# Kernel tuning notes

Hardware: AMD Instinct MI355X
Metric: run time of the kernel (lower is better)

Reference implementation:

```python
import jax, jax.numpy as jnp
import numpy as np

N_CELLS = 50000
HID = 64
DEG = 16
K_NODES = 4  # nodes per cell; cell i owns nodes [4i, 4i+4)
SP = 3


def setup_inputs() -> dict:
    key = jax.random.key(0)
    ks = jax.random.split(key, 12)
    s = 1.0 / np.sqrt(HID)
    inp = {
        'features': jax.random.normal(ks[0], (N_CELLS, HID), jnp.float32),
        'positions': jax.random.normal(ks[1], (K_NODES * N_CELLS, SP), jnp.float32),
        'neighbors': jax.random.randint(ks[2], (N_CELLS, DEG), 0, N_CELLS, jnp.int32),
        # message MLP: Linear(2H+1 -> H), SiLU, Linear(H -> H)
        'W1': jax.random.normal(ks[3], (2 * HID + 1, HID), jnp.float32) * s,
        'b1': jnp.zeros((HID,), jnp.float32),
        'W2': jax.random.normal(ks[4], (HID, HID), jnp.float32) * s,
        'b2': jnp.zeros((HID,), jnp.float32),
        # update MLP: Linear(H + H -> H), SiLU, Linear(H -> H)
        'Wu1': jax.random.normal(ks[5], (2 * HID, HID), jnp.float32) * s,
        'bu1': jnp.zeros((HID,), jnp.float32),
        'Wu2': jax.random.normal(ks[6], (HID, HID), jnp.float32) * s,
        'bu2': jnp.zeros((HID,), jnp.float32),
    }
    return inp


def reference(features, positions, neighbors, W1, b1, W2, b2, Wu1, bu1, Wu2, bu2):
    N, H = features.shape
    # centroid of each cell's owned nodes (cell i -> nodes [K*i, K*i+K))
    cent = positions.reshape(N, K_NODES, SP).mean(axis=1)          # [N, sp]
    fj = features[neighbors]                                       # [N, D, H]
    cj = cent[neighbors]                                           # [N, D, sp]
    # centroid-distance geometric invariant per (cell, neighbor) pair
    geom = jnp.linalg.norm(cent[:, None, :] - cj, axis=-1, keepdims=True)  # [N, D, 1]
    fi = jnp.broadcast_to(features[:, None, :], fj.shape)          # [N, D, H]
    x = jnp.concatenate([fi, fj, geom], axis=-1)                   # [N, D, 2H+1]
    h = jax.nn.silu(x @ W1 + b1) @ W2 + b2                         # [N, D, H]
    msg = h.mean(axis=1)                                           # mean over neighbors
    u = jnp.concatenate([features, msg], axis=-1)                  # [N, 2H]
    upd = jax.nn.silu(u @ Wu1 + bu1) @ Wu2 + bu2
    updated_features = features + upd
    return updated_features, positions
```

## Files before the change

kernel.cpp:

```cpp
#include <hip/hip_runtime.h>


#define DEG 16

typedef __attribute__((ext_vector_type(8))) short short8;
typedef __attribute__((ext_vector_type(4))) float f32x4;
typedef uint2 uint2_a __attribute__((may_alias));
typedef uint4 uint4_a __attribute__((may_alias));
typedef unsigned short ushort_a __attribute__((may_alias));

union HbRd { uint4_a u; short8 s; };
union Frag { short8 s; uint4 u; };

__device__ __forceinline__ unsigned f2bf(float f) {
  unsigned u = __float_as_uint(f);
  return (u + 0x7FFFu + ((u >> 16) & 1u)) >> 16;
}
__device__ __forceinline__ float bf2f(unsigned bits16) {
  return __uint_as_float(bits16 << 16);
}
__device__ __forceinline__ float silu(float h) {
  return h / (1.f + __expf(-h));
}
__device__ __forceinline__ float silu_fast(float h) {
  return h * __builtin_amdgcn_rcpf(1.f + __expf(-h));
}

__global__ __launch_bounds__(256) void prep_aux_kernel(
    const float* __restrict__ feat,
    const float* __restrict__ pos,
    const float* __restrict__ W1, const float* __restrict__ W2,
    const float* __restrict__ Wu1, const float* __restrict__ Wu2,
    float* __restrict__ outpos, float* __restrict__ cent4,
    unsigned short* __restrict__ w1pq, unsigned short* __restrict__ w2t,
    unsigned short* __restrict__ wu1t, unsigned short* __restrict__ wu2b,
    unsigned char* __restrict__ Q8)
{
  __shared__ unsigned short w1q[4096];

  if (blockIdx.x < 782) {
    const int tid  = threadIdx.x;
    const int lane = tid & 63;
    const int wid  = tid >> 6;
    const int quad = lane >> 4;
    const int l15  = lane & 15;

    {
      const int q  = (tid >> 3) & 3;
      const int kk = (tid >> 5) & 1;
      const int mq = tid >> 6;
      #pragma unroll
      for (int u = 0; u < 2; ++u) {
        const int l = (tid * 2 + u) & 15;
        const float* src = W1 + (64 + kk * 32 + q * 8) * 64 + mq * 16 + l;
        unsigned short v[8];
        #pragma unroll
        for (int j = 0; j < 8; ++j)
          v[j] = (unsigned short)f2bf(src[j * 64]);
        uint4 pk;
        pk.x = (unsigned)v[0] | ((unsigned)v[1] << 16);
        pk.y = (unsigned)v[2] | ((unsigned)v[3] << 16);
        pk.z = (unsigned)v[4] | ((unsigned)v[5] << 16);
        pk.w = (unsigned)v[6] | ((unsigned)v[7] << 16);
        ((uint4*)w1q)[tid * 2 + u] = pk;
      }
    }

    const int tile = blockIdx.x * 4 + wid;
    const bool act = (tile < 3125);
    const int  tt  = act ? tile : 3124;
    const int  cr  = tt * 16 + l15;

    short8 xf[2];
    #pragma unroll
    for (int kk = 0; kk < 2; ++kk) {
      const float4 f0 = *(const float4*)(feat + cr * 64 + kk * 32 + quad * 8);
      const float4 f1 = *(const float4*)(feat + cr * 64 + kk * 32 + quad * 8 + 4);
      Frag v;
      v.s[0] = (short)f2bf(f0.x); v.s[1] = (short)f2bf(f0.y);
      v.s[2] = (short)f2bf(f0.z); v.s[3] = (short)f2bf(f0.w);
      v.s[4] = (short)f2bf(f1.x); v.s[5] = (short)f2bf(f1.y);
      v.s[6] = (short)f2bf(f1.z); v.s[7] = (short)f2bf(f1.w);
      xf[kk] = v.s;
    }

    __syncthreads();

    short8 wf[4][2];
    #pragma unroll
    for (int m = 0; m < 4; ++m)
      #pragma unroll
      for (int kk = 0; kk < 2; ++kk)
        wf[m][kk] = *(const short8*)(w1q + (((m * 2 + kk) * 4 + quad) << 7) + l15 * 8);

    f32x4 acc[4] = {};
    #pragma unroll
    for (int kk = 0; kk < 2; ++kk)
      #pragma unroll
      for (int m = 0; m < 4; ++m)
        acc[m] = __builtin_amdgcn_mfma_f32_16x16x32_bf16(wf[m][kk], xf[kk], acc[m], 0, 0, 0);

    if (act) {
      #pragma unroll
      for (int m = 0; m < 4; ++m) {
        int w = __builtin_amdgcn_cvt_pk_fp8_f32(acc[m][0], acc[m][1], 0, false);
        w = __builtin_amdgcn_cvt_pk_fp8_f32(acc[m][2], acc[m][3], w, true);
        *(unsigned int*)(Q8 + cr * 64 + m * 16 + quad * 4) = (unsigned)w;
      }
    }
  } else {
    const int t = (blockIdx.x - 782) * 256 + threadIdx.x;
    if (t < 150000) {
      ((float4*)outpos)[t] = ((const float4*)pos)[t];
    } else if (t < 174576) {
      const int r = t - 150000;
      if (r < 8192) {
        const int j = r & 7, l = (r >> 3) & 15, q = (r >> 7) & 3;
        const int f = r >> 9, kk = f & 1, mt = f >> 1;
        const int k = kk * 32 + q * 8 + j;
        const int m = mt * 16 + l;
        w1pq[r] = (unsigned short)f2bf(
            (m < 64) ? W1[k * 64 + m] : W1[(k + 64) * 64 + (m - 64)]);
      } else if (r < 12288) {
        const int s = r - 8192;
        const int j = s & 7, l = (s >> 3) & 15, q = (s >> 7) & 3;
        const int f = s >> 9, kk = f & 1, mt = f >> 1;
        const int k = kk * 32 + q * 8 + j;
        w2t[s] = (unsigned short)f2bf(W2[k * 64 + mt * 16 + l]);
      } else if (r < 20480) {
        const int s = r - 12288;
        const int j = s & 7, l = (s >> 3) & 15, q = (s >> 7) & 3;
        const int f = s >> 9, kk = f & 3, mt = f >> 2;
        const int k = kk * 32 + q * 8 + j;
        wu1t[s] = (unsigned short)f2bf(Wu1[k * 64 + mt * 16 + l]);
      } else {
        const int s = r - 20480;
        const int j = s & 7, l = (s >> 3) & 15, q = (s >> 7) & 3;
        const int f = s >> 9, kk = f & 1, nt = f >> 1;
        const int k = kk * 32 + q * 8 + j;
        wu2b[s] = (unsigned short)f2bf(Wu2[k * 64 + nt * 16 + l]);
      }
    } else if (t < 224576) {
      const int i = t - 174576;
      const float4* pp = (const float4*)(pos + 12 * i);
      const float4 a = pp[0], b = pp[1], c = pp[2];
      float4 o;
      o.x = (a.x + a.w + b.z + c.y) * 0.25f;
      o.y = (a.y + b.x + b.w + c.z) * 0.25f;
      o.z = (a.z + b.y + c.x + c.w) * 0.25f;
      o.w = 0.f;
      ((float4*)cent4)[i] = o;
    }
  }
}

__global__ __launch_bounds__(256) void msg_tail_kernel(
    const unsigned char* __restrict__ Q8,
    const float4* __restrict__ cent4,
    const int* __restrict__ nbr,
    const float* __restrict__ feat,
    const unsigned short* __restrict__ w1pq,
    const unsigned short* __restrict__ w2t,
    const unsigned short* __restrict__ wu1t,
    const unsigned short* __restrict__ wu2b,
    const float* __restrict__ b1, const float* __restrict__ W1,
    const float* __restrict__ b2, const float* __restrict__ bu1,
    const float* __restrict__ bu2,
    float* __restrict__ outf)
{
  __shared__ uint4 smem[432];
  char* sT  = (char*)smem;
  char* Msg = sT + 2304;
  char* Hb  = sT + 4608;

  const int lane = threadIdx.x & 63;
  const int wid  = threadIdx.x >> 6;
  const int quad = lane >> 4;
  const int l15  = lane & 15;
  const int tile = blockIdx.x;
  const int cr   = tile * 16 + l15;

  const float b1l = b1[lane];
  const float wl  = W1[8192 + lane];

  int nj[4];
  #pragma unroll
  for (int i = 0; i < 4; ++i) {
    const int cs = __builtin_amdgcn_readfirstlane(tile * 16 + wid * 4 + i);
    nj[i] = nbr[cs * DEG + l15];
  }
  float g[4];
  #pragma unroll
  for (int i = 0; i < 4; ++i) {
    const int cs = __builtin_amdgcn_readfirstlane(tile * 16 + wid * 4 + i);
    const float4 ci = cent4[cs];
    const float4 cj = cent4[nj[i]];
    const float dx = ci.x - cj.x, dy = ci.y - cj.y, dz = ci.z - cj.z;
    g[i] = sqrtf(dx * dx + dy * dy + dz * dz);
  }

  Frag xf[2];
  #pragma unroll
  for (int kk = 0; kk < 2; ++kk) {
    const float4 f0 = *(const float4*)(feat + cr * 64 + kk * 32 + quad * 8);
    const float4 f1 = *(const float4*)(feat + cr * 64 + kk * 32 + quad * 8 + 4);
    Frag v;
    v.s[0] = (short)f2bf(f0.x); v.s[1] = (short)f2bf(f0.y);
    v.s[2] = (short)f2bf(f0.z); v.s[3] = (short)f2bf(f0.w);
    v.s[4] = (short)f2bf(f1.x); v.s[5] = (short)f2bf(f1.y);
    v.s[6] = (short)f2bf(f1.z); v.s[7] = (short)f2bf(f1.w);
    xf[kk] = v;
  }

  {
    short8 wpf[2];
    #pragma unroll
    for (int kk = 0; kk < 2; ++kk)
      wpf[kk] = *(const short8*)(w1pq + (((wid * 2 + kk) * 4 + quad) << 7) + l15 * 8);
    f32x4 accp = {};
    #pragma unroll
    for (int kk = 0; kk < 2; ++kk)
      accp = __builtin_amdgcn_mfma_f32_16x16x32_bf16(wpf[kk], xf[kk].s, accp, 0, 0, 0);
    uint2 pk;
    pk.x = f2bf(accp[0]) | (f2bf(accp[1]) << 16);
    pk.y = f2bf(accp[2]) | (f2bf(accp[3]) << 16);
    *(uint2_a*)(sT + l15 * 144 + wid * 32 + quad * 8) = pk;
  }

  unsigned qA[16], qB[16];
  #pragma unroll
  for (int d = 0; d < 16; ++d) {
    const int nd = __builtin_amdgcn_readlane(nj[0], d);
    qA[d] = Q8[nd * 64 + lane];
  }

  __syncthreads();

  #pragma unroll
  for (int i = 0; i < 4; ++i) {
    unsigned (&qc)[16] = (i & 1) ? qB : qA;
    unsigned (&qn)[16] = (i & 1) ? qA : qB;
    if (i < 3) {
      #pragma unroll
      for (int d = 0; d < 16; ++d) {
        const int nd = __builtin_amdgcn_readlane(nj[i + 1], d);
        qn[d] = Q8[nd * 64 + lane];
      }
    }
    const float pcb =
        bf2f(((const ushort_a*)(sT + (wid * 4 + i) * 144))[lane]) + b1l;
    float acc = 0.f;
    #pragma unroll
    for (int d = 0; d < 16; ++d) {
      const float gd = __uint_as_float(
          __builtin_amdgcn_readlane((int)__float_as_uint(g[i]), d));
      const float qv = __builtin_amdgcn_cvt_f32_fp8((int)qc[d], 0);
      acc += silu_fast(pcb + qv + gd * wl);
    }
    ((ushort_a*)(sT + (wid * 4 + i) * 144))[lane] =
        (unsigned short)f2bf(acc * 0.0625f);
  }

  short8 w2f[2], wu1f[4], wu2f[2];
  #pragma unroll
  for (int kk = 0; kk < 2; ++kk)
    w2f[kk]  = *(const short8*)(w2t  + (((wid * 2 + kk) * 4 + quad) << 7) + l15 * 8);
  #pragma unroll
  for (int kk = 0; kk < 4; ++kk)
    wu1f[kk] = *(const short8*)(wu1t + (((wid * 4 + kk) * 4 + quad) << 7) + l15 * 8);
  #pragma unroll
  for (int kk = 0; kk < 2; ++kk)
    wu2f[kk] = *(const short8*)(wu2b + (((wid * 2 + kk) * 4 + quad) << 7) + l15 * 8);

  const f32x4 b2f  = *(const f32x4*)(b2  + wid * 16 + quad * 4);
  const f32x4 bu1f = *(const f32x4*)(bu1 + wid * 16 + quad * 4);
  const float bu2v = bu2[wid * 16 + l15];

  __syncthreads();

  f32x4 accm = {};
  #pragma unroll
  for (int kk = 0; kk < 2; ++kk) {
    HbRd t; t.u = *(const uint4_a*)(sT + l15 * 144 + kk * 64 + quad * 16);
    accm = __builtin_amdgcn_mfma_f32_16x16x32_bf16(w2f[kk], t.s, accm, 0, 0, 0);
  }
  {
    uint2 pk;
    pk.x = f2bf(accm[0] + b2f[0]) | (f2bf(accm[1] + b2f[1]) << 16);
    pk.y = f2bf(accm[2] + b2f[2]) | (f2bf(accm[3] + b2f[3]) << 16);
    *(uint2_a*)(Msg + l15 * 144 + wid * 32 + quad * 8) = pk;
  }
  __syncthreads();

  f32x4 accu = {};
  #pragma unroll
  for (int kk = 0; kk < 4; ++kk) {
    short8 bf;
    if (kk < 2) {
      bf = xf[kk].s;
    } else {
      HbRd t; t.u = *(const uint4_a*)(Msg + l15 * 144 + (kk - 2) * 64 + quad * 16);
      bf = t.s;
    }
    accu = __builtin_amdgcn_mfma_f32_16x16x32_bf16(wu1f[kk], bf, accu, 0, 0, 0);
  }
  {
    float sv[4];
    #pragma unroll
    for (int rg = 0; rg < 4; ++rg)
      sv[rg] = silu(accu[rg] + bu1f[rg]);
    uint2 pk;
    pk.x = f2bf(sv[0]) | (f2bf(sv[1]) << 16);
    pk.y = f2bf(sv[2]) | (f2bf(sv[3]) << 16);
    *(uint2_a*)(Hb + l15 * 144 + wid * 32 + quad * 8) = pk;
  }
  __syncthreads();

  f32x4 acc2 = {};
  #pragma unroll
  for (int kk = 0; kk < 2; ++kk) {
    HbRd t; t.u = *(const uint4_a*)(Hb + l15 * 144 + kk * 64 + quad * 16);
    acc2 = __builtin_amdgcn_mfma_f32_16x16x32_bf16(t.s, wu2f[kk], acc2, 0, 0, 0);
  }
  #pragma unroll
  for (int rg = 0; rg < 4; ++rg) {
    const int row = tile * 16 + quad * 4 + rg;
    const int col = wid * 16 + l15;
    outf[row * 64 + col] = feat[row * 64 + col] + acc2[rg] + bu2v;
  }
}

extern "C" void kernel_launch(void* const* d_in, const int* in_sizes, int n_in,
                              void* d_out, int out_size, void* d_ws, size_t ws_size,
                              hipStream_t stream)
{
  const float* feat = (const float*)d_in[0];
  const float* pos  = (const float*)d_in[1];
  const int*   nbr  = (const int*)d_in[2];
  const float* W1   = (const float*)d_in[3];
  const float* b1   = (const float*)d_in[4];
  const float* W2   = (const float*)d_in[5];
  const float* b2   = (const float*)d_in[6];
  const float* Wu1  = (const float*)d_in[7];
  const float* bu1  = (const float*)d_in[8];
  const float* Wu2  = (const float*)d_in[9];
  const float* bu2  = (const float*)d_in[10];
  float* out = (float*)d_out;

  unsigned char*  Q8    = (unsigned char*)((char*)d_ws + 12800000);
  float*          cent4 = (float*)((char*)d_ws + 25600000);
  unsigned short* w1pq  = (unsigned short*)((char*)d_ws + 26400000);
  unsigned short* w2t   = (unsigned short*)((char*)d_ws + 26416384);
  unsigned short* wu1t  = (unsigned short*)((char*)d_ws + 26424576);
  unsigned short* wu2b  = (unsigned short*)((char*)d_ws + 26440960);

  prep_aux_kernel<<<1660, 256, 0, stream>>>(feat, pos, W1, W2, Wu1, Wu2,
                                            out + 3200000, cent4,
                                            w1pq, w2t, wu1t, wu2b, Q8);
  msg_tail_kernel<<<3125, 256, 0, stream>>>(Q8, (const float4*)cent4, nbr, feat,
                                            w1pq, w2t, wu1t, wu2b,
                                            b1, W1, b2, bu1, bu2, out);
}
```

Measured before the change: 118.7 us.

## Make msg_tail kernel persistent with prefetch of next tile's loads

Converts the message/update kernel into a grid-stride persistent loop over 16-cell tiles, launching 1042 blocks instead of 3125. Weight fragments are loaded once per block and reused across the tiles it processes. The neighbor indices, centroid distances and feature fragments for the next tile are loaded during the current tile's MLP tail to hide global latency. This raises register pressure and reduces the number of resident blocks available to hide latency, and the uneven tile count across blocks may leave a tail imbalance.

```diff
diff --git a/kernel.cpp b/kernel.cpp
--- a/kernel.cpp
+++ b/kernel.cpp
@@ -25,6 +25,38 @@
 __device__ __forceinline__ float silu_fast(float h) {
   return h * __builtin_amdgcn_rcpf(1.f + __expf(-h));
 }
+
+#define EARLY_LOADS(T, NJ, G, XF)                                              \
+  {                                                                            \
+    _Pragma("unroll")                                                          \
+    for (int i_ = 0; i_ < 4; ++i_) {                                           \
+      const int cs_ = __builtin_amdgcn_readfirstlane((T) * 16 + wid * 4 + i_); \
+      NJ[i_] = nbr[cs_ * DEG + l15];                                           \
+    }                                                                          \
+    _Pragma("unroll")                                                          \
+    for (int i_ = 0; i_ < 4; ++i_) {                                           \
+      const int cs_ = __builtin_amdgcn_readfirstlane((T) * 16 + wid * 4 + i_); \
+      const float4 ci_ = cent4c[cs_];                                          \
+      const float4 cj_ = cent4c[NJ[i_]];                                       \
+      const float dx_ = ci_.x - cj_.x, dy_ = ci_.y - cj_.y,                    \
+                  dz_ = ci_.z - cj_.z;                                         \
+      G[i_] = sqrtf(dx_ * dx_ + dy_ * dy_ + dz_ * dz_);                        \
+    }                                                                          \
+    const int crE_ = (T) * 16 + l15;                                           \
+    _Pragma("unroll")                                                          \
+    for (int kk_ = 0; kk_ < 2; ++kk_) {                                        \
+      const float4 f0_ =                                                       \
+          *(const float4*)(feat + crE_ * 64 + kk_ * 32 + quad * 8);            \
+      const float4 f1_ =                                                       \
+          *(const float4*)(feat + crE_ * 64 + kk_ * 32 + quad * 8 + 4);        \
+      Frag v_;                                                                 \
+      v_.s[0] = (short)f2bf(f0_.x); v_.s[1] = (short)f2bf(f0_.y);              \
+      v_.s[2] = (short)f2bf(f0_.z); v_.s[3] = (short)f2bf(f0_.w);              \
+      v_.s[4] = (short)f2bf(f1_.x); v_.s[5] = (short)f2bf(f1_.y);              \
+      v_.s[6] = (short)f2bf(f1_.z); v_.s[7] = (short)f2bf(f1_.w);              \
+      XF[kk_] = v_.s;                                                          \
+    }                                                                          \
+  }
 
 __global__ __launch_bounds__(256) void prep_aux_kernel(
     const float* __restrict__ feat,
@@ -156,7 +188,7 @@
 
 __global__ __launch_bounds__(256) void msg_tail_kernel(
     const unsigned char* __restrict__ Q8,
-    const float4* __restrict__ cent4,
+    const float4* __restrict__ cent4c,
     const int* __restrict__ nbr,
     const float* __restrict__ feat,
     const unsigned short* __restrict__ w1pq,
@@ -177,91 +209,16 @@
   const int wid  = threadIdx.x >> 6;
   const int quad = lane >> 4;
   const int l15  = lane & 15;
-  const int tile = blockIdx.x;
-  const int cr   = tile * 16 + l15;
+  const int bid  = blockIdx.x;
+  const int gdim = gridDim.x;
 
   const float b1l = b1[lane];
   const float wl  = W1[8192 + lane];
 
-  int nj[4];
+  short8 wpf[2], w2f[2], wu1f[4], wu2f[2];
   #pragma unroll
-  for (int i = 0; i < 4; ++i) {
-    const int cs = __builtin_amdgcn_readfirstlane(tile * 16 + wid * 4 + i);
-    nj[i] = nbr[cs * DEG + l15];
-  }
-  float g[4];
-  #pragma unroll
-  for (int i = 0; i < 4; ++i) {
-    const int cs = __builtin_amdgcn_readfirstlane(tile * 16 + wid * 4 + i);
-    const float4 ci = cent4[cs];
-    const float4 cj = cent4[nj[i]];
-    const float dx = ci.x - cj.x, dy = ci.y - cj.y, dz = ci.z - cj.z;
-    g[i] = sqrtf(dx * dx + dy * dy + dz * dz);
-  }
-
-  Frag xf[2];
-  #pragma unroll
-  for (int kk = 0; kk < 2; ++kk) {
-    const float4 f0 = *(const float4*)(feat + cr * 64 + kk * 32 + quad * 8);
-    const float4 f1 = *(const float4*)(feat + cr * 64 + kk * 32 + quad * 8 + 4);
-    Frag v;
-    v.s[0] = (short)f2bf(f0.x); v.s[1] = (short)f2bf(f0.y);
-    v.s[2] = (short)f2bf(f0.z); v.s[3] = (short)f2bf(f0.w);
-    v.s[4] = (short)f2bf(f1.x); v.s[5] = (short)f2bf(f1.y);
-    v.s[6] = (short)f2bf(f1.z); v.s[7] = (short)f2bf(f1.w);
-    xf[kk] = v;
-  }
-
-  {
-    short8 wpf[2];
-    #pragma unroll
-    for (int kk = 0; kk < 2; ++kk)
-      wpf[kk] = *(const short8*)(w1pq + (((wid * 2 + kk) * 4 + quad) << 7) + l15 * 8);
-    f32x4 accp = {};
-    #pragma unroll
-    for (int kk = 0; kk < 2; ++kk)
-      accp = __builtin_amdgcn_mfma_f32_16x16x32_bf16(wpf[kk], xf[kk].s, accp, 0, 0, 0);
-    uint2 pk;
-    pk.x = f2bf(accp[0]) | (f2bf(accp[1]) << 16);
-    pk.y = f2bf(accp[2]) | (f2bf(accp[3]) << 16);
-    *(uint2_a*)(sT + l15 * 144 + wid * 32 + quad * 8) = pk;
-  }
-
-  unsigned qA[16], qB[16];
-  #pragma unroll
-  for (int d = 0; d < 16; ++d) {
-    const int nd = __builtin_amdgcn_readlane(nj[0], d);
-    qA[d] = Q8[nd * 64 + lane];
-  }
-
-  __syncthreads();
-
-  #pragma unroll
-  for (int i = 0; i < 4; ++i) {
-    unsigned (&qc)[16] = (i & 1) ? qB : qA;
-    unsigned (&qn)[16] = (i & 1) ? qA : qB;
-    if (i < 3) {
-      #pragma unroll
-      for (int d = 0; d < 16; ++d) {
-        const int nd = __builtin_amdgcn_readlane(nj[i + 1], d);
-        qn[d] = Q8[nd * 64 + lane];
-      }
-    }
-    const float pcb =
-        bf2f(((const ushort_a*)(sT + (wid * 4 + i) * 144))[lane]) + b1l;
-    float acc = 0.f;
-    #pragma unroll
-    for (int d = 0; d < 16; ++d) {
-      const float gd = __uint_as_float(
-          __builtin_amdgcn_readlane((int)__float_as_uint(g[i]), d));
-      const float qv = __builtin_amdgcn_cvt_f32_fp8((int)qc[d], 0);
-      acc += silu_fast(pcb + qv + gd * wl);
-    }
-    ((ushort_a*)(sT + (wid * 4 + i) * 144))[lane] =
-        (unsigned short)f2bf(acc * 0.0625f);
-  }
-
-  short8 w2f[2], wu1f[4], wu2f[2];
+  for (int kk = 0; kk < 2; ++kk)
+    wpf[kk]  = *(const short8*)(w1pq + (((wid * 2 + kk) * 4 + quad) << 7) + l15 * 8);
   #pragma unroll
   for (int kk = 0; kk < 2; ++kk)
     w2f[kk]  = *(const short8*)(w2t  + (((wid * 2 + kk) * 4 + quad) << 7) + l15 * 8);
@@ -276,57 +233,119 @@
   const f32x4 bu1f = *(const f32x4*)(bu1 + wid * 16 + quad * 4);
   const float bu2v = bu2[wid * 16 + l15];
 
-  __syncthreads();
-
-  f32x4 accm = {};
-  #pragma unroll
-  for (int kk = 0; kk < 2; ++kk) {
-    HbRd t; t.u = *(const uint4_a*)(sT + l15 * 144 + kk * 64 + quad * 16);
-    accm = __builtin_amdgcn_mfma_f32_16x16x32_bf16(w2f[kk], t.s, accm, 0, 0, 0);
-  }
-  {
-    uint2 pk;
-    pk.x = f2bf(accm[0] + b2f[0]) | (f2bf(accm[1] + b2f[1]) << 16);
-    pk.y = f2bf(accm[2] + b2f[2]) | (f2bf(accm[3] + b2f[3]) << 16);
-    *(uint2_a*)(Msg + l15 * 144 + wid * 32 + quad * 8) = pk;
-  }
-  __syncthreads();
-
-  f32x4 accu = {};
-  #pragma unroll
-  for (int kk = 0; kk < 4; ++kk) {
-    short8 bf;
-    if (kk < 2) {
-      bf = xf[kk].s;
-    } else {
-      HbRd t; t.u = *(const uint4_a*)(Msg + l15 * 144 + (kk - 2) * 64 + quad * 16);
-      bf = t.s;
-    }
-    accu = __builtin_amdgcn_mfma_f32_16x16x32_bf16(wu1f[kk], bf, accu, 0, 0, 0);
-  }
-  {
-    float sv[4];
-    #pragma unroll
-    for (int rg = 0; rg < 4; ++rg)
-      sv[rg] = silu(accu[rg] + bu1f[rg]);
-    uint2 pk;
-    pk.x = f2bf(sv[0]) | (f2bf(sv[1]) << 16);
-    pk.y = f2bf(sv[2]) | (f2bf(sv[3]) << 16);
-    *(uint2_a*)(Hb + l15 * 144 + wid * 32 + quad * 8) = pk;
-  }
-  __syncthreads();
-
-  f32x4 acc2 = {};
-  #pragma unroll
-  for (int kk = 0; kk < 2; ++kk) {
-    HbRd t; t.u = *(const uint4_a*)(Hb + l15 * 144 + kk * 64 + quad * 16);
-    acc2 = __builtin_amdgcn_mfma_f32_16x16x32_bf16(t.s, wu2f[kk], acc2, 0, 0, 0);
-  }
-  #pragma unroll
-  for (int rg = 0; rg < 4; ++rg) {
-    const int row = tile * 16 + quad * 4 + rg;
-    const int col = wid * 16 + l15;
-    outf[row * 64 + col] = feat[row * 64 + col] + acc2[rg] + bu2v;
+  int nj[4]; float g[4]; short8 xf[2];
+  EARLY_LOADS(bid, nj, g, xf);
+
+  for (int tile = bid; tile < 3125; tile += gdim) {
+    {
+      f32x4 accp = {};
+      #pragma unroll
+      for (int kk = 0; kk < 2; ++kk)
+        accp = __builtin_amdgcn_mfma_f32_16x16x32_bf16(wpf[kk], xf[kk], accp, 0, 0, 0);
+      uint2 pk;
+      pk.x = f2bf(accp[0]) | (f2bf(accp[1]) << 16);
+      pk.y = f2bf(accp[2]) | (f2bf(accp[3]) << 16);
+      *(uint2_a*)(sT + l15 * 144 + wid * 32 + quad * 8) = pk;
+    }
+
+    unsigned qA[16], qB[16];
+    #pragma unroll
+    for (int d = 0; d < 16; ++d) {
+      const int nd = __builtin_amdgcn_readlane(nj[0], d);
+      qA[d] = Q8[nd * 64 + lane];
+    }
+
+    __syncthreads();
+
+    #pragma unroll
+    for (int i = 0; i < 4; ++i) {
+      unsigned (&qc)[16] = (i & 1) ? qB : qA;
+      unsigned (&qn)[16] = (i & 1) ? qA : qB;
+      if (i < 3) {
+        #pragma unroll
+        for (int d = 0; d < 16; ++d) {
+          const int nd = __builtin_amdgcn_readlane(nj[i + 1], d);
+          qn[d] = Q8[nd * 64 + lane];
+        }
+      }
+      const float pcb =
+          bf2f(((const ushort_a*)(sT + (wid * 4 + i) * 144))[lane]) + b1l;
+      float acc = 0.f;
+      #pragma unroll
+      for (int d = 0; d < 16; ++d) {
+        const float gd = __uint_as_float(
+            __builtin_amdgcn_readlane((int)__float_as_uint(g[i]), d));
+        const float qv = __builtin_amdgcn_cvt_f32_fp8((int)qc[d], 0);
+        acc += silu_fast(pcb + qv + gd * wl);
+      }
+      ((ushort_a*)(sT + (wid * 4 + i) * 144))[lane] =
+          (unsigned short)f2bf(acc * 0.0625f);
+    }
+
+    __syncthreads();
+
+    int nj2[4]; float g2[4]; short8 xf2[2];
+    const int tn = tile + gdim;
+    if (tn < 3125) EARLY_LOADS(tn, nj2, g2, xf2);
+
+    {
+      f32x4 accm = {};
+      #pragma unroll
+      for (int kk = 0; kk < 2; ++kk) {
+        HbRd t; t.u = *(const uint4_a*)(sT + l15 * 144 + kk * 64 + quad * 16);
+        accm = __builtin_amdgcn_mfma_f32_16x16x32_bf16(w2f[kk], t.s, accm, 0, 0, 0);
+      }
+      uint2 pk;
+      pk.x = f2bf(accm[0] + b2f[0]) | (f2bf(accm[1] + b2f[1]) << 16);
+      pk.y = f2bf(accm[2] + b2f[2]) | (f2bf(accm[3] + b2f[3]) << 16);
+      *(uint2_a*)(Msg + l15 * 144 + wid * 32 + quad * 8) = pk;
+    }
+    __syncthreads();
+
+    {
+      f32x4 accu = {};
+      #pragma unroll
+      for (int kk = 0; kk < 4; ++kk) {
+        short8 bf;
+        if (kk < 2) {
+          bf = xf[kk];
+        } else {
+          HbRd t; t.u = *(const uint4_a*)(Msg + l15 * 144 + (kk - 2) * 64 + quad * 16);
+          bf = t.s;
+        }
+        accu = __builtin_amdgcn_mfma_f32_16x16x32_bf16(wu1f[kk], bf, accu, 0, 0, 0);
+      }
+      float sv[4];
+      #pragma unroll
+      for (int rg = 0; rg < 4; ++rg)
+        sv[rg] = silu(accu[rg] + bu1f[rg]);
+      uint2 pk;
+      pk.x = f2bf(sv[0]) | (f2bf(sv[1]) << 16);
+      pk.y = f2bf(sv[2]) | (f2bf(sv[3]) << 16);
+      *(uint2_a*)(Hb + l15 * 144 + wid * 32 + quad * 8) = pk;
+    }
+    __syncthreads();
+
+    {
+      f32x4 acc2 = {};
+      #pragma unroll
+      for (int kk = 0; kk < 2; ++kk) {
+        HbRd t; t.u = *(const uint4_a*)(Hb + l15 * 144 + kk * 64 + quad * 16);
+        acc2 = __builtin_amdgcn_mfma_f32_16x16x32_bf16(t.s, wu2f[kk], acc2, 0, 0, 0);
+      }
+      #pragma unroll
+      for (int rg = 0; rg < 4; ++rg) {
+        const int row = tile * 16 + quad * 4 + rg;
+        const int col = wid * 16 + l15;
+        outf[row * 64 + col] = feat[row * 64 + col] + acc2[rg] + bu2v;
+      }
+    }
+
+    if (tn < 3125) {
+      #pragma unroll
+      for (int i = 0; i < 4; ++i) { nj[i] = nj2[i]; g[i] = g2[i]; }
+      xf[0] = xf2[0]; xf[1] = xf2[1];
+    }
   }
 }
 
@@ -357,7 +376,7 @@
   prep_aux_kernel<<<1660, 256, 0, stream>>>(feat, pos, W1, W2, Wu1, Wu2,
                                             out + 3200000, cent4,
                                             w1pq, w2t, wu1t, wu2b, Q8);
-  msg_tail_kernel<<<3125, 256, 0, stream>>>(Q8, (const float4*)cent4, nbr, feat,
+  msg_tail_kernel<<<1042, 256, 0, stream>>>(Q8, (const float4*)cent4, nbr, feat,
                                             w1pq, w2t, wu1t, wu2b,
                                             b1, W1, b2, bu1, bu2, out);
 }
```

Measured after the change: 132.6 us. 11.7% more time.
